# Kernel tuning notes

Hardware: AMD Instinct MI355X
Metric: run time of the kernel (lower is better)

Reference implementation:

```python
import jax, jax.numpy as jnp
import numpy as np

N = 1_000_000
C_IN = 64
COORD_SHIFT = 1024  # keeps shifted coords non-negative (offsets are small)


def setup_inputs() -> dict:
    key = jax.random.key(0)
    ks = jax.random.split(key, 8)
    feats = jax.random.normal(ks[0], (N, C_IN), dtype=jnp.float32)
    coords = jax.random.randint(ks[1], (N, 4), 0, 2048, dtype=jnp.int32)
    mask = jnp.ones((N,), dtype=bool)
    # Pointwise decoder params per decoder_blocks [(64,32),(32,16),(16,3)], bias=True
    s1, s2, s3 = 1.0 / np.sqrt(C_IN), 1.0 / np.sqrt(32), 1.0 / np.sqrt(16)
    W1 = jax.random.normal(ks[2], (C_IN, 32), dtype=jnp.float32) * s1
    b1 = jnp.zeros((32,), dtype=jnp.float32)
    W2 = jax.random.normal(ks[3], (32, 16), dtype=jnp.float32) * s2
    b2 = jnp.zeros((16,), dtype=jnp.float32)
    W3 = jax.random.normal(ks[4], (16, 3), dtype=jnp.float32) * s3
    b3 = jnp.zeros((3,), dtype=jnp.float32)
    return {"feats": feats, "coords": coords, "mask": mask,
            "W1": W1, "b1": b1, "W2": W2, "b2": b2, "W3": W3, "b3": b3}


def _decode(feats, mask, W1, b1, W2, b2, W3, b3):
    # FeatDecoder reduced to its pointwise (kernel-size-1 equivalent) form.
    h = jax.nn.relu(feats @ W1 + b1)
    h = jax.nn.relu(h @ W2 + b2)
    offsets = h @ W3 + b3  # [N, 3]
    return offsets * mask[:, None].astype(offsets.dtype)


def _revoxelize(offsets, coords):
    # offsets_ = [0 | round(offsets)] added to original coords
    off_i = jnp.round(offsets).astype(jnp.int32)                 # [N,3]
    new_coords = coords.at[:, 1:].add(off_i)                     # [N,4]
    # sphash -> unique -> sphashquery == row-wise unique with inverse map
    shifted = new_coords + COORD_SHIFT                           # non-negative rows
    _, inv = jnp.unique(shifted, axis=0, size=N, fill_value=0,
                        return_inverse=True)                      # inv: [N]
    inv = inv.reshape(-1).astype(jnp.int32)
    # spcount: voxels per cluster
    counts = jax.ops.segment_sum(jnp.ones((N,), jnp.float32), inv, num_segments=N)
    # spvoxelize: per-cluster mean of shifted coords, then .int()
    sums = jax.ops.segment_sum(new_coords.astype(jnp.float32), inv, num_segments=N)
    out_coords = (sums / jnp.maximum(counts, 1.0)[:, None]).astype(jnp.int32)
    return out_coords, inv


def reference(feats, coords, mask, W1, b1, W2, b2, W3, b3):
    offsets = _decode(feats, mask, W1, b1, W2, b2, W3, b3)
    out_coords, inv_map = _revoxelize(offsets, coords)
    return offsets, out_coords, inv_map
```

## Files before the change

### kernel.cpp

```cpp
#include <hip/hip_runtime.h>
#include <hip/hip_bf16.h>
#include <stdint.h>


#define TPB 256
#define NB 139264
#define NCHUNK 544
typedef unsigned long long ull;

__global__ __launch_bounds__(256) void k_mlp(
    const float* __restrict__ feats, const int* __restrict__ coords,
    const unsigned char* __restrict__ mask,
    const float* __restrict__ W1, const float* __restrict__ b1,
    const float* __restrict__ W2, const float* __restrict__ b2,
    const float* __restrict__ W3, const float* __restrict__ b3,
    float* __restrict__ out_off, ull* __restrict__ slots,
    unsigned int* __restrict__ cursor, int n)
{
    __shared__ float sW1[2048];
    __shared__ float sW2[512];
    __shared__ float sW3[48];
    __shared__ float sb1[32];
    __shared__ float sb2[16];
    __shared__ float sb3[3];
    for (int t = threadIdx.x; t < 2048; t += TPB) sW1[t] = W1[t];
    for (int t = threadIdx.x; t < 512;  t += TPB) sW2[t] = W2[t];
    if (threadIdx.x < 48) sW3[threadIdx.x] = W3[threadIdx.x];
    if (threadIdx.x < 32) sb1[threadIdx.x] = b1[threadIdx.x];
    if (threadIdx.x < 16) sb2[threadIdx.x] = b2[threadIdx.x];
    if (threadIdx.x < 3)  sb3[threadIdx.x] = b3[threadIdx.x];
    __syncthreads();

    int i = blockIdx.x * TPB + threadIdx.x;
    if (i >= n) return;

    float h1[32];
    #pragma unroll
    for (int j = 0; j < 32; ++j) h1[j] = 0.0f;
    const float4* f4 = (const float4*)(feats + (size_t)i * 64);
    #pragma unroll
    for (int kc = 0; kc < 16; ++kc) {
        float4 xv = f4[kc];
        #pragma unroll
        for (int d = 0; d < 4; ++d) {
            float x = (d == 0) ? xv.x : (d == 1) ? xv.y : (d == 2) ? xv.z : xv.w;
            const float* wr = &sW1[(kc * 4 + d) * 32];
            #pragma unroll
            for (int j = 0; j < 32; j += 4) {
                float4 w = *(const float4*)(wr + j);
                h1[j + 0] = fmaf(x, w.x, h1[j + 0]);
                h1[j + 1] = fmaf(x, w.y, h1[j + 1]);
                h1[j + 2] = fmaf(x, w.z, h1[j + 2]);
                h1[j + 3] = fmaf(x, w.w, h1[j + 3]);
            }
        }
    }
    #pragma unroll
    for (int j = 0; j < 32; ++j) h1[j] = fmaxf(h1[j] + sb1[j], 0.0f);

    float h2[16];
    #pragma unroll
    for (int j = 0; j < 16; ++j) h2[j] = 0.0f;
    #pragma unroll
    for (int k = 0; k < 32; ++k) {
        float x = h1[k];
        const float* wr = &sW2[k * 16];
        #pragma unroll
        for (int j = 0; j < 16; j += 4) {
            float4 w = *(const float4*)(wr + j);
            h2[j + 0] = fmaf(x, w.x, h2[j + 0]);
            h2[j + 1] = fmaf(x, w.y, h2[j + 1]);
            h2[j + 2] = fmaf(x, w.z, h2[j + 2]);
            h2[j + 3] = fmaf(x, w.w, h2[j + 3]);
        }
    }
    #pragma unroll
    for (int j = 0; j < 16; ++j) h2[j] = fmaxf(h2[j] + sb2[j], 0.0f);

    float o0 = 0.0f, o1 = 0.0f, o2 = 0.0f;
    #pragma unroll
    for (int k = 0; k < 16; ++k) {
        float x = h2[k];
        o0 = fmaf(x, sW3[k * 3 + 0], o0);
        o1 = fmaf(x, sW3[k * 3 + 1], o1);
        o2 = fmaf(x, sW3[k * 3 + 2], o2);
    }
    o0 += sb3[0]; o1 += sb3[1]; o2 += sb3[2];

    float m = mask[i] ? 1.0f : 0.0f;
    o0 *= m; o1 *= m; o2 *= m;
    out_off[(size_t)3 * i + 0] = o0;
    out_off[(size_t)3 * i + 1] = o1;
    out_off[(size_t)3 * i + 2] = o2;

    int4 c = ((const int4*)coords)[i];
    int r1 = (int)rintf(o0), r2 = (int)rintf(o1), r3 = (int)rintf(o2);
    int c1u = c.y + r1, c2u = c.z + r2, c3u = c.w + r3;
    int c1s = min(max(c1u + 1024, 0), 8191);
    int c2s = min(max(c2u + 1024, 0), 8191);
    int c3s = min(max(c3u + 1024, 0), 8191);
    int bin1 = min(max((c1u + 64) >> 5, 0), 67);
    int b = c.x * 68 + bin1;
    ull row39 = ((ull)c1s << 26) | ((ull)c2s << 13) | (ull)c3s;
    ull packed = (row39 << 20) | (ull)(unsigned int)i;
    unsigned int j = atomicAdd(&cursor[b], 1u);
    if (j < 64u) slots[(size_t)b * 64 + j] = packed;
}

__device__ inline ull wave_sort64(ull v, int lane)
{
    #pragma unroll
    for (int k = 2; k <= 64; k <<= 1) {
        #pragma unroll
        for (int j = k >> 1; j > 0; j >>= 1) {
            ull o = __shfl_xor(v, j, 64);
            bool up = ((lane & k) == 0);
            bool lower = ((lane & j) == 0);
            ull mn = (v < o) ? v : o;
            ull mx = (v < o) ? o : v;
            v = (up == lower) ? mn : mx;
        }
    }
    return v;
}

__global__ __launch_bounds__(256) void k_passA(
    const ull* __restrict__ slots, const unsigned int* __restrict__ cursor,
    unsigned int* __restrict__ ucnt)
{
    int lane = threadIdx.x & 63;
    int b = blockIdx.x * 4 + (threadIdx.x >> 6);
    unsigned int cnt = cursor[b];
    if (cnt > 64u) cnt = 64u;
    if (cnt == 0u) { if (lane == 0) ucnt[b] = 0u; return; }
    ull v = (lane < (int)cnt) ? slots[(size_t)b * 64 + lane] : ~0ULL;
    v = wave_sort64(v, lane);
    ull row = v >> 20;
    ull prev = __shfl_up(row, 1, 64);
    bool head = (lane < (int)cnt) && ((lane == 0) || (row != prev));
    ull hm = __ballot(head);
    if (lane == 0) ucnt[b] = (unsigned int)__popcll(hm);
}

__global__ __launch_bounds__(256) void k_scanA(
    const unsigned int* __restrict__ ucnt, unsigned int* __restrict__ lstart,
    unsigned int* __restrict__ chsum)
{
    __shared__ unsigned int s[256];
    int tid = threadIdx.x;
    int g = blockIdx.x * 256 + tid;
    unsigned int v = ucnt[g];
    s[tid] = v;
    __syncthreads();
    for (int ofs = 1; ofs < 256; ofs <<= 1) {
        unsigned int t = (tid >= ofs) ? s[tid - ofs] : 0u;
        __syncthreads();
        s[tid] += t;
        __syncthreads();
    }
    lstart[g] = s[tid] - v;
    if (tid == 255) chsum[blockIdx.x] = s[255];
}

__global__ __launch_bounds__(1024) void k_scanB(unsigned int* __restrict__ chsum)
{
    __shared__ unsigned int s[1024];
    int tid = threadIdx.x;
    unsigned int v = (tid < NCHUNK) ? chsum[tid] : 0u;
    s[tid] = v;
    __syncthreads();
    for (int ofs = 1; ofs < 1024; ofs <<= 1) {
        unsigned int t = (tid >= ofs) ? s[tid - ofs] : 0u;
        __syncthreads();
        s[tid] += t;
        __syncthreads();
    }
    if (tid < NCHUNK) chsum[tid] = s[tid] - v;
}

__global__ __launch_bounds__(256) void k_passB(
    const ull* __restrict__ slots, const unsigned int* __restrict__ cursor,
    const unsigned int* __restrict__ lstart, const unsigned int* __restrict__ chbase,
    float* __restrict__ out_oc, float* __restrict__ out_inv)
{
    int lane = threadIdx.x & 63;
    int b = blockIdx.x * 4 + (threadIdx.x >> 6);
    unsigned int cnt = cursor[b];
    if (cnt > 64u) cnt = 64u;
    if (cnt == 0u) return;
    ull v = (lane < (int)cnt) ? slots[(size_t)b * 64 + lane] : ~0ULL;
    v = wave_sort64(v, lane);
    ull row = v >> 20;
    unsigned int idx = (unsigned int)(v & 0xFFFFFULL);
    ull prev = __shfl_up(row, 1, 64);
    bool head = (lane < (int)cnt) && ((lane == 0) || (row != prev));
    ull hm = __ballot(head);
    ull le = (lane == 63) ? ~0ULL : ((1ULL << (lane + 1)) - 1ULL);
    int lrank = __popcll(hm & le) - 1;
    unsigned int base = chbase[b >> 8] + lstart[b];
    unsigned int r = base + (unsigned int)lrank;
    if (lane < (int)cnt) out_inv[idx] = (float)r;

    int c3s = (int)(row & 0x1FFFULL);
    int c2s = (int)((row >> 13) & 0x1FFFULL);
    int c1s = (int)(row >> 26);
    ull sum = (lane < (int)cnt)
        ? ((1ULL << 57) | ((ull)c1s << 38) | ((ull)c2s << 19) | (ull)c3s)
        : 0ULL;
    ull P = sum;
    #pragma unroll
    for (int d = 1; d < 64; d <<= 1) {
        ull t = __shfl_up(P, d, 64);
        if (lane >= d) P += t;
    }
    ull gt = hm & ~le;
    int tpos = gt ? (__ffsll((long long)gt) - 2) : ((int)cnt - 1);
    ull Pt = __shfl(P, tpos, 64);
    int hsrc = (lane > 0) ? lane - 1 : 0;
    ull Ph = __shfl(P, hsrc, 64);
    if (lane == 0) Ph = 0ULL;
    if (head) {
        ull run = Pt - Ph;
        int rc = (int)(run >> 57);
        int s1 = (int)((run >> 38) & 0x7FFFFULL) - 1024 * rc;
        int s2 = (int)((run >> 19) & 0x7FFFFULL) - 1024 * rc;
        int s3 = (int)(run & 0x7FFFFULL) - 1024 * rc;
        float fc = (float)rc;
        float4 o;
        o.x = (float)((unsigned int)b / 68u);
        o.y = truncf((float)s1 / fc);
        o.z = truncf((float)s2 / fc);
        o.w = truncf((float)s3 / fc);
        ((float4*)out_oc)[r] = o;
    }
}

extern "C" void kernel_launch(void* const* d_in, const int* in_sizes, int n_in,
                              void* d_out, int out_size, void* d_ws, size_t ws_size,
                              hipStream_t stream)
{
    const float*         feats  = (const float*)d_in[0];
    const int*           coords = (const int*)d_in[1];
    const unsigned char* mask   = (const unsigned char*)d_in[2];
    const float* W1 = (const float*)d_in[3];
    const float* b1 = (const float*)d_in[4];
    const float* W2 = (const float*)d_in[5];
    const float* b2 = (const float*)d_in[6];
    const float* W3 = (const float*)d_in[7];
    const float* b3 = (const float*)d_in[8];

    int n = in_sizes[1] / 4;

    char* ws = (char*)d_ws;
    ull*          slots  = (ull*)ws;
    unsigned int* cursor = (unsigned int*)(ws + (size_t)NB * 64 * 8);
    unsigned int* ucnt   = cursor + NB;
    unsigned int* lstart = ucnt + NB;
    unsigned int* chsum  = lstart + NB;

    float* out     = (float*)d_out;
    float* out_off = out;
    float* out_oc  = out + (size_t)3 * n;
    float* out_inv = out + (size_t)7 * n;

    hipMemsetAsync(cursor, 0, (size_t)NB * sizeof(unsigned int), stream);
    hipMemsetAsync(out_oc, 0, (size_t)4 * n * sizeof(float), stream);

    int nb256 = (n + TPB - 1) / TPB;

    k_mlp<<<nb256, TPB, 0, stream>>>(feats, coords, mask, W1, b1, W2, b2, W3, b3,
                                     out_off, slots, cursor, n);
    k_passA<<<NB / 4, TPB, 0, stream>>>(slots, cursor, ucnt);
    k_scanA<<<NCHUNK, 256, 0, stream>>>(ucnt, lstart, chsum);
    k_scanB<<<1, 1024, 0, stream>>>(chsum);
    k_passB<<<NB / 4, TPB, 0, stream>>>(slots, cursor, lstart, chsum, out_oc, out_inv);
}
```

Baseline: 594.6 us.

## Sort buckets once, store run sums, and fix up ranks in lightweight passes

The bucket sort, head detection and segmented coordinate sums now happen once, in the first pass. That pass writes per-run packed sums back into the slots and a provisional bucket-local rank into the inverse map. Two light kernels then add global offsets: one rewrites the inverse map and one computes the per-cluster mean coordinates. This removes the second full bitonic sort of every bucket. The sort width is also chosen by bucket occupancy, and MLP weights are read directly from global memory instead of being staged in LDS, which drops the per-block copy and barrier but depends on cache and scalar loads for the weights.

```diff
diff --git a/kernel.cpp b/kernel.cpp
--- a/kernel.cpp
+++ b/kernel.cpp
@@ -17,34 +17,21 @@
     float* __restrict__ out_off, ull* __restrict__ slots,
     unsigned int* __restrict__ cursor, int n)
 {
-    __shared__ float sW1[2048];
-    __shared__ float sW2[512];
-    __shared__ float sW3[48];
-    __shared__ float sb1[32];
-    __shared__ float sb2[16];
-    __shared__ float sb3[3];
-    for (int t = threadIdx.x; t < 2048; t += TPB) sW1[t] = W1[t];
-    for (int t = threadIdx.x; t < 512;  t += TPB) sW2[t] = W2[t];
-    if (threadIdx.x < 48) sW3[threadIdx.x] = W3[threadIdx.x];
-    if (threadIdx.x < 32) sb1[threadIdx.x] = b1[threadIdx.x];
-    if (threadIdx.x < 16) sb2[threadIdx.x] = b2[threadIdx.x];
-    if (threadIdx.x < 3)  sb3[threadIdx.x] = b3[threadIdx.x];
-    __syncthreads();
-
     int i = blockIdx.x * TPB + threadIdx.x;
     if (i >= n) return;
 
+    const float4* f4 = (const float4*)(feats + (size_t)i * 64);
+
     float h1[32];
     #pragma unroll
     for (int j = 0; j < 32; ++j) h1[j] = 0.0f;
-    const float4* f4 = (const float4*)(feats + (size_t)i * 64);
     #pragma unroll
     for (int kc = 0; kc < 16; ++kc) {
         float4 xv = f4[kc];
         #pragma unroll
         for (int d = 0; d < 4; ++d) {
             float x = (d == 0) ? xv.x : (d == 1) ? xv.y : (d == 2) ? xv.z : xv.w;
-            const float* wr = &sW1[(kc * 4 + d) * 32];
+            const float* wr = W1 + (kc * 4 + d) * 32;
             #pragma unroll
             for (int j = 0; j < 32; j += 4) {
                 float4 w = *(const float4*)(wr + j);
@@ -56,7 +43,7 @@
         }
     }
     #pragma unroll
-    for (int j = 0; j < 32; ++j) h1[j] = fmaxf(h1[j] + sb1[j], 0.0f);
+    for (int j = 0; j < 32; ++j) h1[j] = fmaxf(h1[j] + b1[j], 0.0f);
 
     float h2[16];
     #pragma unroll
@@ -64,7 +51,7 @@
     #pragma unroll
     for (int k = 0; k < 32; ++k) {
         float x = h1[k];
-        const float* wr = &sW2[k * 16];
+        const float* wr = W2 + k * 16;
         #pragma unroll
         for (int j = 0; j < 16; j += 4) {
             float4 w = *(const float4*)(wr + j);
@@ -75,17 +62,17 @@
         }
     }
     #pragma unroll
-    for (int j = 0; j < 16; ++j) h2[j] = fmaxf(h2[j] + sb2[j], 0.0f);
+    for (int j = 0; j < 16; ++j) h2[j] = fmaxf(h2[j] + b2[j], 0.0f);
 
     float o0 = 0.0f, o1 = 0.0f, o2 = 0.0f;
     #pragma unroll
     for (int k = 0; k < 16; ++k) {
         float x = h2[k];
-        o0 = fmaf(x, sW3[k * 3 + 0], o0);
-        o1 = fmaf(x, sW3[k * 3 + 1], o1);
-        o2 = fmaf(x, sW3[k * 3 + 2], o2);
-    }
-    o0 += sb3[0]; o1 += sb3[1]; o2 += sb3[2];
+        o0 = fmaf(x, W3[k * 3 + 0], o0);
+        o1 = fmaf(x, W3[k * 3 + 1], o1);
+        o2 = fmaf(x, W3[k * 3 + 2], o2);
+    }
+    o0 += b3[0]; o1 += b3[1]; o2 += b3[2];
 
     float m = mask[i] ? 1.0f : 0.0f;
     o0 *= m; o1 *= m; o2 *= m;
@@ -107,14 +94,15 @@
     if (j < 64u) slots[(size_t)b * 64 + j] = packed;
 }
 
-__device__ inline ull wave_sort64(ull v, int lane)
-{
-    #pragma unroll
-    for (int k = 2; k <= 64; k <<= 1) {
+template<int W>
+__device__ inline ull seg_sort(ull v, int lane)
+{
+    #pragma unroll
+    for (int k = 2; k <= W; k <<= 1) {
         #pragma unroll
         for (int j = k >> 1; j > 0; j >>= 1) {
             ull o = __shfl_xor(v, j, 64);
-            bool up = ((lane & k) == 0);
+            bool up = ((lane & (k & (W - 1))) == 0);
             bool lower = ((lane & j) == 0);
             ull mn = (v < o) ? v : o;
             ull mx = (v < o) ? o : v;
@@ -125,8 +113,8 @@
 }
 
 __global__ __launch_bounds__(256) void k_passA(
-    const ull* __restrict__ slots, const unsigned int* __restrict__ cursor,
-    unsigned int* __restrict__ ucnt)
+    ull* __restrict__ slots, const unsigned int* __restrict__ cursor,
+    unsigned int* __restrict__ ucnt, float* __restrict__ out_inv)
 {
     int lane = threadIdx.x & 63;
     int b = blockIdx.x * 4 + (threadIdx.x >> 6);
@@ -134,12 +122,41 @@
     if (cnt > 64u) cnt = 64u;
     if (cnt == 0u) { if (lane == 0) ucnt[b] = 0u; return; }
     ull v = (lane < (int)cnt) ? slots[(size_t)b * 64 + lane] : ~0ULL;
-    v = wave_sort64(v, lane);
+    if      (cnt <= 8u)  v = seg_sort<8>(v, lane);
+    else if (cnt <= 16u) v = seg_sort<16>(v, lane);
+    else if (cnt <= 32u) v = seg_sort<32>(v, lane);
+    else                 v = seg_sort<64>(v, lane);
+
     ull row = v >> 20;
+    unsigned int idx = (unsigned int)(v & 0xFFFFFULL);
     ull prev = __shfl_up(row, 1, 64);
     bool head = (lane < (int)cnt) && ((lane == 0) || (row != prev));
     ull hm = __ballot(head);
+    ull le = (lane == 63) ? ~0ULL : ((1ULL << (lane + 1)) - 1ULL);
+    int lrank = __popcll(hm & le) - 1;
     if (lane == 0) ucnt[b] = (unsigned int)__popcll(hm);
+    if (lane < (int)cnt)
+        ((unsigned int*)out_inv)[idx] = (unsigned int)(b * 64 + lrank);
+
+    int c3s = (int)(row & 0x1FFFULL);
+    int c2s = (int)((row >> 13) & 0x1FFFULL);
+    int c1s = (int)(row >> 26);
+    ull sum = (lane < (int)cnt)
+        ? ((1ULL << 57) | ((ull)c1s << 38) | ((ull)c2s << 19) | (ull)c3s)
+        : 0ULL;
+    ull P = sum;
+    #pragma unroll
+    for (int d = 1; d < 64; d <<= 1) {
+        ull t = __shfl_up(P, d, 64);
+        if (lane >= d) P += t;
+    }
+    ull gt = hm & ~le;
+    int tpos = gt ? (__ffsll((long long)gt) - 2) : ((int)cnt - 1);
+    ull Pt = __shfl(P, tpos, 64);
+    int hsrc = (lane > 0) ? lane - 1 : 0;
+    ull Ph = __shfl(P, hsrc, 64);
+    if (lane == 0) Ph = 0ULL;
+    if (head) slots[(size_t)b * 64 + lrank] = Pt - Ph;
 }
 
 __global__ __launch_bounds__(256) void k_scanA(
@@ -178,61 +195,40 @@
     if (tid < NCHUNK) chsum[tid] = s[tid] - v;
 }
 
-__global__ __launch_bounds__(256) void k_passB(
-    const ull* __restrict__ slots, const unsigned int* __restrict__ cursor,
+__global__ __launch_bounds__(256) void k_fixinv(
+    float* __restrict__ out_inv, const unsigned int* __restrict__ lstart,
+    const unsigned int* __restrict__ chbase, int n)
+{
+    int i = blockIdx.x * TPB + threadIdx.x;
+    if (i >= n) return;
+    unsigned int q = ((const unsigned int*)out_inv)[i];
+    unsigned int b = q >> 6, lr = q & 63u;
+    if (b >= NB) b = NB - 1;
+    out_inv[i] = (float)(chbase[b >> 8] + lstart[b] + lr);
+}
+
+__global__ __launch_bounds__(256) void k_fixout(
+    const ull* __restrict__ slots, const unsigned int* __restrict__ ucnt,
     const unsigned int* __restrict__ lstart, const unsigned int* __restrict__ chbase,
-    float* __restrict__ out_oc, float* __restrict__ out_inv)
+    float* __restrict__ out_oc)
 {
     int lane = threadIdx.x & 63;
     int b = blockIdx.x * 4 + (threadIdx.x >> 6);
-    unsigned int cnt = cursor[b];
-    if (cnt > 64u) cnt = 64u;
-    if (cnt == 0u) return;
-    ull v = (lane < (int)cnt) ? slots[(size_t)b * 64 + lane] : ~0ULL;
-    v = wave_sort64(v, lane);
-    ull row = v >> 20;
-    unsigned int idx = (unsigned int)(v & 0xFFFFFULL);
-    ull prev = __shfl_up(row, 1, 64);
-    bool head = (lane < (int)cnt) && ((lane == 0) || (row != prev));
-    ull hm = __ballot(head);
-    ull le = (lane == 63) ? ~0ULL : ((1ULL << (lane + 1)) - 1ULL);
-    int lrank = __popcll(hm & le) - 1;
-    unsigned int base = chbase[b >> 8] + lstart[b];
-    unsigned int r = base + (unsigned int)lrank;
-    if (lane < (int)cnt) out_inv[idx] = (float)r;
-
-    int c3s = (int)(row & 0x1FFFULL);
-    int c2s = (int)((row >> 13) & 0x1FFFULL);
-    int c1s = (int)(row >> 26);
-    ull sum = (lane < (int)cnt)
-        ? ((1ULL << 57) | ((ull)c1s << 38) | ((ull)c2s << 19) | (ull)c3s)
-        : 0ULL;
-    ull P = sum;
-    #pragma unroll
-    for (int d = 1; d < 64; d <<= 1) {
-        ull t = __shfl_up(P, d, 64);
-        if (lane >= d) P += t;
-    }
-    ull gt = hm & ~le;
-    int tpos = gt ? (__ffsll((long long)gt) - 2) : ((int)cnt - 1);
-    ull Pt = __shfl(P, tpos, 64);
-    int hsrc = (lane > 0) ? lane - 1 : 0;
-    ull Ph = __shfl(P, hsrc, 64);
-    if (lane == 0) Ph = 0ULL;
-    if (head) {
-        ull run = Pt - Ph;
-        int rc = (int)(run >> 57);
-        int s1 = (int)((run >> 38) & 0x7FFFFULL) - 1024 * rc;
-        int s2 = (int)((run >> 19) & 0x7FFFFULL) - 1024 * rc;
-        int s3 = (int)(run & 0x7FFFFULL) - 1024 * rc;
-        float fc = (float)rc;
-        float4 o;
-        o.x = (float)((unsigned int)b / 68u);
-        o.y = truncf((float)s1 / fc);
-        o.z = truncf((float)s2 / fc);
-        o.w = truncf((float)s3 / fc);
-        ((float4*)out_oc)[r] = o;
-    }
+    unsigned int uc = ucnt[b];
+    if (lane >= (int)uc) return;
+    ull run = slots[(size_t)b * 64 + lane];
+    unsigned int r = chbase[b >> 8] + lstart[b] + (unsigned int)lane;
+    int rc = (int)(run >> 57);
+    int s1 = (int)((run >> 38) & 0x7FFFFULL) - 1024 * rc;
+    int s2 = (int)((run >> 19) & 0x7FFFFULL) - 1024 * rc;
+    int s3 = (int)(run & 0x7FFFFULL) - 1024 * rc;
+    float fc = (float)rc;
+    float4 o;
+    o.x = (float)((unsigned int)b / 68u);
+    o.y = truncf((float)s1 / fc);
+    o.z = truncf((float)s2 / fc);
+    o.w = truncf((float)s3 / fc);
+    ((float4*)out_oc)[r] = o;
 }
 
 extern "C" void kernel_launch(void* const* d_in, const int* in_sizes, int n_in,
@@ -270,8 +266,9 @@
 
     k_mlp<<<nb256, TPB, 0, stream>>>(feats, coords, mask, W1, b1, W2, b2, W3, b3,
                                      out_off, slots, cursor, n);
-    k_passA<<<NB / 4, TPB, 0, stream>>>(slots, cursor, ucnt);
+    k_passA<<<NB / 4, TPB, 0, stream>>>(slots, cursor, ucnt, out_inv);
     k_scanA<<<NCHUNK, 256, 0, stream>>>(ucnt, lstart, chsum);
     k_scanB<<<1, 1024, 0, stream>>>(chsum);
-    k_passB<<<NB / 4, TPB, 0, stream>>>(slots, cursor, lstart, chsum, out_oc, out_inv);
-}
+    k_fixinv<<<nb256, TPB, 0, stream>>>(out_inv, lstart, chsum, n);
+    k_fixout<<<NB / 4, TPB, 0, stream>>>(slots, ucnt, lstart, chsum, out_oc);
+}
```

Result: faster. 543.0 us (-8.7%).
